# Performance work log

Hardware: AMD Instinct MI355X
Metric: run time of the kernel (lower is better)

The kernel has to match this reference:

```python
import jax, jax.numpy as jnp
import numpy as np

EPS = 1e-6


def _min_max_norm(v):
    # torch: 2.0 + (v - v.min()) / (v.max() - v.min()), global scalars
    mn, mx = v.min(), v.max()
    return 2.0 + (v - mn) / (mx - mn)


def setup_inputs() -> dict:
    key = jax.random.key(0)
    k1, k2, k3 = jax.random.split(key, 3)
    B, C, H, W = 2, 32, 96, 128
    return {
        "queries": jax.random.normal(k1, (B, C, H, W), jnp.float32),
        "keys": jax.random.normal(k2, (B, C, H, W), jnp.float32),
        "values": jax.random.normal(k3, (B, C, H, W), jnp.float32),
    }


def reference(queries, keys, values):
    B, C, H, W = queries.shape

    def row_column_softmax(s):  # s: [B,C,H,W]
        rc = jax.nn.softmax(s, axis=3) + jax.nn.softmax(s, axis=2)
        return rc / rc.max()

    def per_channel(q_c):  # q_c: [B,H,W] -> one output channel
        q = jnp.broadcast_to(q_c[:, None], (B, C, H, W))  # repeat over C
        # q_k_transpose: [B,C,H,H] (einsum sums w and y independently)
        hxh = jnp.einsum('bchw,bcxy->bchx', q, keys) + EPS
        # q_transpose_k: [B,C,W,W]
        wxw = jnp.einsum('bchw,bcxy->bcwy', q, keys) + EPS
        h_row = _min_max_norm(hxh.sum(axis=2))  # [B,C,H]  ('bcij->bcj')
        h_col = _min_max_norm(hxh.sum(axis=3))  # [B,C,H]  ('bcij->bci')
        w_row = _min_max_norm(wxw.sum(axis=2))  # [B,C,W]
        w_col = _min_max_norm(wxw.sum(axis=3))  # [B,C,W]
        outer = lambda m, n: jnp.einsum('bch,bcw->bchw', m, n)
        score = (row_column_softmax(outer(h_row, w_row))
                 + row_column_softmax(outer(h_row, w_col))
                 + row_column_softmax(outer(h_col, w_row))
                 + row_column_softmax(outer(h_col, w_col)))
        score = score / score.max()
        z_c = jnp.einsum('bchw,bchw->bhw', score, values)  # [B,H,W]
        return z_c, score

    # vectorize the original Python loop over query channels
    z_all, scores = jax.vmap(per_channel)(jnp.moveaxis(queries, 1, 0))
    z = jnp.swapaxes(z_all, 0, 1)  # [B,C,H,W]
    # torch returns the atten_score of the LAST loop iteration
    return z, scores[-1]
```

## Files before the change

### kernel.cpp

```cpp
#include <hip/hip_runtime.h>
#include <float.h>

#define BB 2
#define CC 32
#define HH 96
#define WW 128
#define HW (HH*WW)
#define BC (BB*CC)
#define NPLANE (BC*HW)
#define EPSF 1e-6f
#define LOG2E 1.4426950408889634f

#define QR_OFF 0
#define QC_OFF (QR_OFF + BC*HH)
#define QS_OFF (QC_OFF + BC*WW)
#define KR_OFF (QS_OFF + BC)
#define KC_OFF (KR_OFF + BC*HH)
#define KS_OFF (KC_OFF + BC*WW)
#define REC_OFF (KS_OFF + BC)
#define RECSZ 1344
#define BMX_OFF (REC_OFF + CC*BC*RECSZ)
#define BSX_OFF (BMX_OFF + CC*BC*4)

__device__ __forceinline__ float rcpf(float x) { return __builtin_amdgcn_rcpf(x); }
__device__ __forceinline__ float e2(float x) { return __builtin_amdgcn_exp2f(x); }

typedef _Float16 h2v __attribute__((ext_vector_type(2)));
__device__ __forceinline__ unsigned pkrtz_u(float a, float b) {
  return __builtin_bit_cast(unsigned, __builtin_amdgcn_cvt_pkrtz(a, b));
}
__device__ __forceinline__ unsigned pk_add(unsigned a, unsigned b) {
  unsigned d; asm("v_pk_add_f16 %0, %1, %2" : "=v"(d) : "v"(a), "v"(b)); return d;
}
__device__ __forceinline__ unsigned pk_mul(unsigned a, unsigned b) {
  unsigned d; asm("v_pk_mul_f16 %0, %1, %2" : "=v"(d) : "v"(a), "v"(b)); return d;
}
__device__ __forceinline__ unsigned pk_max(unsigned a, unsigned b) {
  unsigned d; asm("v_pk_max_f16 %0, %1, %2" : "=v"(d) : "v"(a), "v"(b)); return d;
}
__device__ __forceinline__ float dot2acc(unsigned u, float acc) {
#if __has_builtin(__builtin_amdgcn_fdot2)
  h2v a = __builtin_bit_cast(h2v, u);
  h2v one = {(_Float16)1.0f, (_Float16)1.0f};
  return __builtin_amdgcn_fdot2(a, one, acc, false);
#else
  float lo = (float)__builtin_bit_cast(_Float16, (unsigned short)(u & 0xffff));
  float hi = (float)__builtin_bit_cast(_Float16, (unsigned short)(u >> 16));
  return acc + lo + hi;
#endif
}
__device__ __forceinline__ float h2max_f(unsigned u) {
  float lo = (float)__builtin_bit_cast(_Float16, (unsigned short)(u & 0xffff));
  float hi = (float)__builtin_bit_cast(_Float16, (unsigned short)(u >> 16));
  return fmaxf(lo, hi);
}

__device__ __forceinline__ float blkmax4(float v) {
  __shared__ float sred[4];
  #pragma unroll
  for (int o = 32; o > 0; o >>= 1) v = fmaxf(v, __shfl_xor(v, o, 64));
  if ((threadIdx.x & 63) == 0) sred[threadIdx.x >> 6] = v;
  __syncthreads();
  float r = fmaxf(fmaxf(sred[0], sred[1]), fmaxf(sred[2], sred[3]));
  __syncthreads();
  return r;
}

__global__ __launch_bounds__(256) void k1_plane_sums(const float* __restrict__ q,
                                                     const float* __restrict__ k,
                                                     float* __restrict__ ws) {
  int pb = blockIdx.x;
  int plane = pb & (BC - 1);
  const float* src = (pb < BC ? q : k) + (size_t)plane * HW;
  float* rowO = ws + (pb < BC ? QR_OFF : KR_OFF) + plane * HH;
  float* colO = ws + (pb < BC ? QC_OFF : KC_OFF) + plane * WW;
  float* totO = ws + (pb < BC ? QS_OFF : KS_OFF) + plane;
  __shared__ float cp[4 * WW];
  __shared__ float rsh[HH];
  __shared__ float wtot[2];
  int tid = threadIdx.x;
  int u = tid >> 6, l = tid & 63;
  float csum0 = 0.f, csum1 = 0.f;
  #pragma unroll 4
  for (int r = 0; r < 24; ++r) {
    int h = u * 24 + r;
    float v0 = src[h * WW + l];
    float v1 = src[h * WW + l + 64];
    csum0 += v0; csum1 += v1;
    float rs = v0 + v1;
    #pragma unroll
    for (int o = 1; o < 64; o <<= 1) rs += __shfl_xor(rs, o, 64);
    if (l == 0) { rowO[h] = rs; rsh[h] = rs; }
  }
  cp[u * WW + l] = csum0;
  cp[u * WW + l + 64] = csum1;
  __syncthreads();
  if (tid < WW) colO[tid] = cp[tid] + cp[WW + tid] + cp[2 * WW + tid] + cp[3 * WW + tid];
  float tv = (tid < HH) ? rsh[tid] : 0.f;
  if (tid < 128) {
    #pragma unroll
    for (int o = 1; o < 64; o <<= 1) tv += __shfl_xor(tv, o, 64);
    if ((tid & 63) == 0) wtot[tid >> 6] = tv;
  }
  __syncthreads();
  if (tid == 0) *totO = wtot[0] + wtot[1];
}

__device__ __forceinline__ float k2_raw(const float* __restrict__ ws, int type, int c0, int i, int L) {
  int bc = i / L, x = i - bc * L;
  int b = bc >> 5;
  if (type == 0) return ws[QS_OFF + b * CC + c0] * ws[KR_OFF + bc * HH + x] + HH * EPSF;
  if (type == 1) return ws[QR_OFF + (b * CC + c0) * HH + x] * ws[KS_OFF + bc] + HH * EPSF;
  if (type == 2) return ws[QS_OFF + b * CC + c0] * ws[KC_OFF + bc * WW + x] + WW * EPSF;
  return ws[QC_OFF + (b * CC + c0) * WW + x] * ws[KS_OFF + bc] + WW * EPSF;
}

__global__ __launch_bounds__(256) void k2_vec_norm(float* __restrict__ ws) {
  int c0 = blockIdx.x >> 2, type = blockIdx.x & 3;
  int L = (type < 2) ? HH : WW;
  int N = BC * L;
  int tid = threadIdx.x;
  float mx = -FLT_MAX, mn = FLT_MAX;
  for (int i = tid; i < N; i += 256) {
    float v = k2_raw(ws, type, c0, i, L);
    mx = fmaxf(mx, v); mn = fminf(mn, v);
  }
  mx = blkmax4(mx);
  mn = -blkmax4(-mn);
  float scale = rcpf(mx - mn);
  float fold = (type < 2) ? LOG2E : 1.0f;
  int fieldbase = (type == 0) ? 0 : (type == 1) ? 96 : (type == 2) ? 192 : 320;
  for (int i = tid; i < N; i += 256) {
    int bc = i / L, x = i - bc * L;
    float v = k2_raw(ws, type, c0, i, L);
    ws[REC_OFF + (size_t)(c0 * BC + bc) * RECSZ + fieldbase + x] =
        (2.0f + (v - mn) * scale) * fold;
  }
}

#define EPH 136
__global__ __launch_bounds__(256) void k3_rc(float* __restrict__ ws) {
  int g = blockIdx.x;
  int vb = g >> 2, t = g & 3;
  float* rec = ws + REC_OFF + (size_t)vb * RECSZ;
  int tid = threadIdx.x;
  int u = tid >> 6, l = tid & 63;
  __shared__ __align__(16) unsigned short eh[HH * EPH];
  __shared__ __align__(16) float mncp[512];
  __shared__ __align__(16) unsigned short rch[128];
  __shared__ float wmx[3];
  const float* mv = rec + (t >> 1) * 96;
  const float* nv = rec + 192 + (t & 1) * 128;
  if (tid < 224) mncp[tid] = (tid < 96) ? mv[tid] : nv[tid - 96];
  __syncthreads();
  float n0 = mncp[96 + 2 * l], n1 = mncp[96 + 2 * l + 1];
  float cs0 = 0.f, cs1 = 0.f;
  #pragma unroll 6
  for (int r = 0; r < 24; ++r) {
    int h = u * 24 + r;
    float m = mncp[h];
    float e0 = e2(m * n0);
    float e1 = e2(m * n1);
    cs0 += e0; cs1 += e1;
    *(unsigned*)&eh[h * EPH + 2 * l] = pkrtz_u(e0, e1);
  }
  __syncthreads();
  mncp[u * 128 + 2 * l] = cs0;
  mncp[u * 128 + 2 * l + 1] = cs1;
  __syncthreads();
  if (tid < 64) {
    int w0 = 2 * tid, w1 = w0 + 1;
    float rc0 = rcpf(mncp[w0] + mncp[128 + w0] + mncp[256 + w0] + mncp[384 + w0]);
    float rc1 = rcpf(mncp[w1] + mncp[128 + w1] + mncp[256 + w1] + mncp[384 + w1]);
    rec[832 + 4 * w0 + t] = rc0;
    rec[832 + 4 * w1 + t] = rc1;
    ((unsigned*)rch)[tid] = pkrtz_u(rc0 * 4096.f, rc1 * 4096.f);
  }
  __syncthreads();
  float mx = 0.f;
  if (tid < 192) {
    int row = tid >> 1, hf = tid & 1;
    const uint4* ep = (const uint4*)&eh[row * EPH + hf * 64];
    float s = 0.f;
    #pragma unroll
    for (int j = 0; j < 8; ++j) {
      uint4 ev = ep[j];
      s = dot2acc(ev.x, s); s = dot2acc(ev.y, s);
      s = dot2acc(ev.z, s); s = dot2acc(ev.w, s);
    }
    s += __shfl_xor(s, 1, 64);
    float rr = rcpf(s);
    if (hf == 0) rec[448 + 4 * row + t] = rr;
    unsigned rr2 = pkrtz_u(rr * 4096.f, rr * 4096.f);
    unsigned mxu = 0;
    const uint4* cp2 = (const uint4*)&rch[hf * 64];
    #pragma unroll
    for (int j = 0; j < 8; ++j) {
      uint4 ev = ep[j];
      uint4 cv = cp2[j];
      mxu = pk_max(mxu, pk_mul(ev.x, pk_add(cv.x, rr2)));
      mxu = pk_max(mxu, pk_mul(ev.y, pk_add(cv.y, rr2)));
      mxu = pk_max(mxu, pk_mul(ev.z, pk_add(cv.z, rr2)));
      mxu = pk_max(mxu, pk_mul(ev.w, pk_add(cv.w, rr2)));
    }
    mx = h2max_f(mxu) * (1.0f / 4096.f);
    #pragma unroll
    for (int o = 1; o < 64; o <<= 1) mx = fmaxf(mx, __shfl_xor(mx, o, 64));
    if ((tid & 63) == 0) wmx[tid >> 6] = mx;
  }
  __syncthreads();
  if (tid == 0) ws[BMX_OFF + vb * 4 + t] = fmaxf(fmaxf(wmx[0], wmx[1]), wmx[2]);
}

#define ELEMS 2
#define TILES 24
#define GRP 4
__global__ __launch_bounds__(256) void k4_score(const float* __restrict__ values,
                                                float* __restrict__ ws,
                                                float* __restrict__ out) {
  int bx = blockIdx.x;
  int tile = bx % TILES;
  int cb = bx / TILES;
  int b = cb & 1, c0 = cb >> 1;
  int tid = threadIdx.x;
  int base = tile * 512;
  int w = tid & 127;
  __shared__ __align__(16) float nS[GRP][256];
  __shared__ __align__(16) float c4S[GRP][512];
  __shared__ __align__(16) float mrf[CC * 24];
  __shared__ float s44[4][4];
  const float* rec0 = ws + REC_OFF + (size_t)(c0 * BC + b * CC) * RECSZ;
  float bm = ws[BMX_OFF + c0 * 256 + tid];
  #pragma unroll
  for (int o = 4; o <= 32; o <<= 1) bm = fmaxf(bm, __shfl_xor(bm, o, 64));
  if ((tid & 63) < 4) s44[tid >> 6][tid & 3] = bm;
  if (tid < 192) {
    int ch = tid / 6, f = tid - 6 * (tid / 6);
    const float* rsrc = rec0 + (size_t)ch * RECSZ;
    int soff = (f == 0) ? tile * 4 : (f == 1) ? 96 + tile * 4 : 448 + 16 * tile + 4 * (f - 2);
    *(float4*)&mrf[ch * 24 + f * 4] = *(const float4*)(rsrc + soff);
  }
  const float* vsrc0 = values + (size_t)(b * CC) * HW + base + tid;
  float v0 = vsrc0[0], v1 = vsrc0[256];
  __syncthreads();
  float im0 = rcpf(fmaxf(fmaxf(s44[0][0], s44[1][0]), fmaxf(s44[2][0], s44[3][0])));
  float im1 = rcpf(fmaxf(fmaxf(s44[0][1], s44[1][1]), fmaxf(s44[2][1], s44[3][1])));
  float im2 = rcpf(fmaxf(fmaxf(s44[0][2], s44[1][2]), fmaxf(s44[2][2], s44[3][2])));
  float im3 = rcpf(fmaxf(fmaxf(s44[0][3], s44[1][3]), fmaxf(s44[2][3], s44[3][3])));
  for (int i = tid; i < CC * 16; i += 256) {
    int ch = i >> 4, kk = i & 15, tt = kk & 3;
    float sel = tt == 0 ? im0 : tt == 1 ? im1 : tt == 2 ? im2 : im3;
    mrf[ch * 24 + 8 + kk] *= sel;
  }
  #pragma unroll
  for (int i = tid; i < GRP * 192; i += 256) {
    int chl = i / 192, rem = i - 192 * (i / 192);
    const float* rsrc = rec0 + (size_t)chl * RECSZ;
    if (rem < 64) {
      *(float4*)&nS[chl][4 * rem] = *(const float4*)(rsrc + 192 + 4 * rem);
    } else {
      float4 g4 = *(const float4*)(rsrc + 832 + 4 * (rem - 64));
      g4.x *= im0; g4.y *= im1; g4.z *= im2; g4.w *= im3;
      *(float4*)&c4S[chl][4 * (rem - 64)] = g4;
    }
  }
  __syncthreads();
  int r0 = tid >> 7;
  float U0 = 0.f, U1 = 0.f, smaxl = 0.f;
  for (int c = 0; c < CC; ++c) {
    if ((c & (GRP - 1)) == 0 && c) {
      __syncthreads();
      #pragma unroll
      for (int i = tid; i < GRP * 192; i += 256) {
        int chl = i / 192, rem = i - 192 * (i / 192);
        const float* rsrc = rec0 + (size_t)(c + chl) * RECSZ;
        if (rem < 64) {
          *(float4*)&nS[chl][4 * rem] = *(const float4*)(rsrc + 192 + 4 * rem);
        } else {
          float4 g4 = *(const float4*)(rsrc + 832 + 4 * (rem - 64));
          g4.x *= im0; g4.y *= im1; g4.z *= im2; g4.w *= im3;
          *(float4*)&c4S[chl][4 * (rem - 64)] = g4;
        }
      }
      __syncthreads();
    }
    float nv0 = 0.f, nv1 = 0.f;
    if (c + 1 < CC) {
      nv0 = vsrc0[(size_t)(c + 1) * HW];
      nv1 = vsrc0[(size_t)(c + 1) * HW + 256];
    }
    int cl = c & (GRP - 1);
    float nr = nS[cl][w], nc = nS[cl][128 + w];
    float4 c4 = *(const float4*)&c4S[cl][4 * w];
    const float* mc = &mrf[c * 24];
    #pragma unroll
    for (int j = 0; j < ELEMS; ++j) {
      int r = r0 + 2 * j;
      float mR = mc[r], mC = mc[4 + r];
      float4 r4 = *(const float4*)&mc[8 + 4 * r];
      float sc = e2(mR * nr) * (r4.x + c4.x) + e2(mR * nc) * (r4.y + c4.y)
               + e2(mC * nr) * (r4.z + c4.z) + e2(mC * nc) * (r4.w + c4.w);
      smaxl = fmaxf(smaxl, sc);
      float uv = sc * (j == 0 ? v0 : v1);
      if (j == 0) U0 += uv; else U1 += uv;
    }
    v0 = nv0; v1 = nv1;
  }
  float* zout = out + (size_t)(b * CC + c0) * HW + base + tid;
  zout[0] = U0;
  zout[256] = U1;
  smaxl = blkmax4(smaxl);
  if (tid == 0) ws[BSX_OFF + bx] = smaxl;
}

#define K5_ZB (BC * 8)
__global__ __launch_bounds__(256) void k5_final(float* __restrict__ out,
                                                const float* __restrict__ ws) {
  int bx = blockIdx.x;
  int tid = threadIdx.x;
  if (bx < K5_ZB) {
    int p = bx >> 3, sub = bx & 7;
    int c0 = p & (CC - 1);
    __shared__ float sm;
    if (tid < 64) {
      float a = (tid < 48) ? ws[BSX_OFF + c0 * 48 + tid] : 0.f;
      #pragma unroll
      for (int o = 1; o < 64; o <<= 1) a = fmaxf(a, __shfl_xor(a, o, 64));
      if (tid == 0) sm = a;
    }
    __syncthreads();
    float ism = rcpf(sm);
    int off = p * HW + sub * 1536 + tid;
    #pragma unroll
    for (int j = 0; j < 6; ++j) out[off + 256 * j] *= ism;
  } else {
    int sp = bx - K5_ZB;
    int plane = sp >> 1, half = sp & 1;
    const float* rec = ws + REC_OFF + (size_t)((CC - 1) * BC + plane) * RECSZ;
    __shared__ __align__(16) float R[RECSZ];
    __shared__ float s44[4][4];
    __shared__ float sm;
    for (int i = tid; i < RECSZ / 4; i += 256) ((float4*)R)[i] = ((const float4*)rec)[i];
    float bm = ws[BMX_OFF + (CC - 1) * 256 + tid];
    #pragma unroll
    for (int o = 4; o <= 32; o <<= 1) bm = fmaxf(bm, __shfl_xor(bm, o, 64));
    if ((tid & 63) < 4) s44[tid >> 6][tid & 3] = bm;
    if (tid < 64) {
      float a = (tid < 48) ? ws[BSX_OFF + (CC - 1) * 48 + tid] : 0.f;
      #pragma unroll
      for (int o = 1; o < 64; o <<= 1) a = fmaxf(a, __shfl_xor(a, o, 64));
      if (tid == 0) sm = a;
    }
    __syncthreads();
    float im0 = rcpf(fmaxf(fmaxf(s44[0][0], s44[1][0]), fmaxf(s44[2][0], s44[3][0])));
    float im1 = rcpf(fmaxf(fmaxf(s44[0][1], s44[1][1]), fmaxf(s44[2][1], s44[3][1])));
    float im2 = rcpf(fmaxf(fmaxf(s44[0][2], s44[1][2]), fmaxf(s44[2][2], s44[3][2])));
    float im3 = rcpf(fmaxf(fmaxf(s44[0][3], s44[1][3]), fmaxf(s44[2][3], s44[3][3])));
    float isml = rcpf(sm);
    float* sout = out + (size_t)NPLANE + (size_t)plane * HW + half * 6144;
    #pragma unroll 4
    for (int e = tid; e < 6144; e += 256) {
      int idx = half * 6144 + e;
      int h = idx >> 7, ww = idx & 127;
      float mR = R[h], mC = R[96 + h];
      float nr = R[192 + ww], nc = R[320 + ww];
      float4 r4 = *(const float4*)&R[448 + 4 * h];
      float4 c4 = *(const float4*)&R[832 + 4 * ww];
      float A0 = c4.x * im0, A1 = c4.y * im1, A2 = c4.z * im2, A3 = c4.w * im3;
      float sc = e2(mR * nr) * fmaf(r4.x, im0, A0) + e2(mR * nc) * fmaf(r4.y, im1, A1)
               + e2(mC * nr) * fmaf(r4.z, im2, A2) + e2(mC * nc) * fmaf(r4.w, im3, A3);
      sout[e] = sc * isml;
    }
  }
}

extern "C" void kernel_launch(void* const* d_in, const int* in_sizes, int n_in,
                              void* d_out, int out_size, void* d_ws, size_t ws_size,
                              hipStream_t stream) {
  const float* q = (const float*)d_in[0];
  const float* k = (const float*)d_in[1];
  const float* v = (const float*)d_in[2];
  float* out = (float*)d_out;
  float* ws = (float*)d_ws;
  k1_plane_sums<<<2 * BC, 256, 0, stream>>>(q, k, ws);
  k2_vec_norm<<<CC * 4, 256, 0, stream>>>(ws);
  k3_rc<<<CC * BC * 4, 256, 0, stream>>>(ws);
  k4_score<<<CC * BB * TILES, 256, 0, stream>>>(v, ws, out);
  k5_final<<<K5_ZB + 128, 256, 0, stream>>>(out, ws);
}
```

Measured before the change: 99.83 us.

## Split k4 channel reduction in two groups with wider pixel tiles per block

k4_score now gives each block half of the 32 value channels and twice as many pixels (four elements per thread instead of two). The grid size stays the same. The second channel group writes its partial z into workspace, and k5_final adds it to the first group's result before scaling by the global max. The aim is to halve the serial channel loop and the LDS refills per block, and to reuse each loaded column factor across four rows for more instruction-level parallelism. The cost is an extra full-size global write and read of partial sums, plus more registers per thread.

```diff
diff --git a/kernel.cpp b/kernel.cpp
--- a/kernel.cpp
+++ b/kernel.cpp
@@ -21,6 +21,7 @@
 #define RECSZ 1344
 #define BMX_OFF (REC_OFF + CC*BC*RECSZ)
 #define BSX_OFF (BMX_OFF + CC*BC*4)
+#define PZ_OFF (BSX_OFF + 1536)
 
 __device__ __forceinline__ float rcpf(float x) { return __builtin_amdgcn_rcpf(x); }
 __device__ __forceinline__ float e2(float x) { return __builtin_amdgcn_exp2f(x); }
@@ -212,50 +213,58 @@
   if (tid == 0) ws[BMX_OFF + vb * 4 + t] = fmaxf(fmaxf(wmx[0], wmx[1]), wmx[2]);
 }
 
-#define ELEMS 2
-#define TILES 24
+#define ELEMS 4
+#define TILES 12
+#define NCG 2
+#define CG (CC/NCG)
 #define GRP 4
 __global__ __launch_bounds__(256) void k4_score(const float* __restrict__ values,
                                                 float* __restrict__ ws,
                                                 float* __restrict__ out) {
   int bx = blockIdx.x;
-  int tile = bx % TILES;
-  int cb = bx / TILES;
+  int cg = bx & 1, bxx = bx >> 1;
+  int tile = bxx % TILES;
+  int cb = bxx / TILES;
   int b = cb & 1, c0 = cb >> 1;
   int tid = threadIdx.x;
-  int base = tile * 512;
-  int w = tid & 127;
+  int base = tile * 1024;
+  int w = tid & 127, r0 = tid >> 7;
   __shared__ __align__(16) float nS[GRP][256];
   __shared__ __align__(16) float c4S[GRP][512];
-  __shared__ __align__(16) float mrf[CC * 24];
+  __shared__ __align__(16) float mrf[CG * 48];
   __shared__ float s44[4][4];
   const float* rec0 = ws + REC_OFF + (size_t)(c0 * BC + b * CC) * RECSZ;
+  const float* recg = rec0 + (size_t)(cg * CG) * RECSZ;
   float bm = ws[BMX_OFF + c0 * 256 + tid];
   #pragma unroll
   for (int o = 4; o <= 32; o <<= 1) bm = fmaxf(bm, __shfl_xor(bm, o, 64));
   if ((tid & 63) < 4) s44[tid >> 6][tid & 3] = bm;
   if (tid < 192) {
-    int ch = tid / 6, f = tid - 6 * (tid / 6);
-    const float* rsrc = rec0 + (size_t)ch * RECSZ;
-    int soff = (f == 0) ? tile * 4 : (f == 1) ? 96 + tile * 4 : 448 + 16 * tile + 4 * (f - 2);
-    *(float4*)&mrf[ch * 24 + f * 4] = *(const float4*)(rsrc + soff);
+    int ch = tid / 12, f = tid - 12 * (tid / 12);
+    const float* rsrc = recg + (size_t)ch * RECSZ;
+    int soff = (f < 2) ? tile * 8 + 4 * f
+             : (f < 4) ? 96 + tile * 8 + 4 * (f - 2)
+                       : 448 + 32 * tile + 4 * (f - 4);
+    *(float4*)&mrf[ch * 48 + f * 4] = *(const float4*)(rsrc + soff);
   }
   const float* vsrc0 = values + (size_t)(b * CC) * HW + base + tid;
-  float v0 = vsrc0[0], v1 = vsrc0[256];
+  float vr[ELEMS];
+  #pragma unroll
+  for (int j = 0; j < ELEMS; ++j) vr[j] = vsrc0[(size_t)(cg * CG) * HW + 256 * j];
   __syncthreads();
   float im0 = rcpf(fmaxf(fmaxf(s44[0][0], s44[1][0]), fmaxf(s44[2][0], s44[3][0])));
   float im1 = rcpf(fmaxf(fmaxf(s44[0][1], s44[1][1]), fmaxf(s44[2][1], s44[3][1])));
   float im2 = rcpf(fmaxf(fmaxf(s44[0][2], s44[1][2]), fmaxf(s44[2][2], s44[3][2])));
   float im3 = rcpf(fmaxf(fmaxf(s44[0][3], s44[1][3]), fmaxf(s44[2][3], s44[3][3])));
-  for (int i = tid; i < CC * 16; i += 256) {
-    int ch = i >> 4, kk = i & 15, tt = kk & 3;
+  for (int i = tid; i < CG * 32; i += 256) {
+    int ch = i >> 5, kk = i & 31, tt = kk & 3;
     float sel = tt == 0 ? im0 : tt == 1 ? im1 : tt == 2 ? im2 : im3;
-    mrf[ch * 24 + 8 + kk] *= sel;
+    mrf[ch * 48 + 16 + kk] *= sel;
   }
   #pragma unroll
   for (int i = tid; i < GRP * 192; i += 256) {
     int chl = i / 192, rem = i - 192 * (i / 192);
-    const float* rsrc = rec0 + (size_t)chl * RECSZ;
+    const float* rsrc = recg + (size_t)chl * RECSZ;
     if (rem < 64) {
       *(float4*)&nS[chl][4 * rem] = *(const float4*)(rsrc + 192 + 4 * rem);
     } else {
@@ -265,15 +274,15 @@
     }
   }
   __syncthreads();
-  int r0 = tid >> 7;
-  float U0 = 0.f, U1 = 0.f, smaxl = 0.f;
-  for (int c = 0; c < CC; ++c) {
-    if ((c & (GRP - 1)) == 0 && c) {
+  float U[ELEMS] = {0.f, 0.f, 0.f, 0.f};
+  float smaxl = 0.f;
+  for (int ci = 0; ci < CG; ++ci) {
+    if ((ci & (GRP - 1)) == 0 && ci) {
       __syncthreads();
       #pragma unroll
       for (int i = tid; i < GRP * 192; i += 256) {
         int chl = i / 192, rem = i - 192 * (i / 192);
-        const float* rsrc = rec0 + (size_t)(c + chl) * RECSZ;
+        const float* rsrc = recg + (size_t)(ci + chl) * RECSZ;
         if (rem < 64) {
           *(float4*)&nS[chl][4 * rem] = *(const float4*)(rsrc + 192 + 4 * rem);
         } else {
@@ -284,31 +293,34 @@
       }
       __syncthreads();
     }
-    float nv0 = 0.f, nv1 = 0.f;
-    if (c + 1 < CC) {
-      nv0 = vsrc0[(size_t)(c + 1) * HW];
-      nv1 = vsrc0[(size_t)(c + 1) * HW + 256];
-    }
-    int cl = c & (GRP - 1);
+    float nv[ELEMS];
+    if (ci + 1 < CG) {
+      #pragma unroll
+      for (int j = 0; j < ELEMS; ++j)
+        nv[j] = vsrc0[(size_t)(cg * CG + ci + 1) * HW + 256 * j];
+    }
+    int cl = ci & (GRP - 1);
     float nr = nS[cl][w], nc = nS[cl][128 + w];
     float4 c4 = *(const float4*)&c4S[cl][4 * w];
-    const float* mc = &mrf[c * 24];
+    const float* mc = &mrf[ci * 48];
     #pragma unroll
     for (int j = 0; j < ELEMS; ++j) {
       int r = r0 + 2 * j;
-      float mR = mc[r], mC = mc[4 + r];
-      float4 r4 = *(const float4*)&mc[8 + 4 * r];
+      float mR = mc[r], mC = mc[8 + r];
+      float4 r4 = *(const float4*)&mc[16 + 4 * r];
       float sc = e2(mR * nr) * (r4.x + c4.x) + e2(mR * nc) * (r4.y + c4.y)
                + e2(mC * nr) * (r4.z + c4.z) + e2(mC * nc) * (r4.w + c4.w);
       smaxl = fmaxf(smaxl, sc);
-      float uv = sc * (j == 0 ? v0 : v1);
-      if (j == 0) U0 += uv; else U1 += uv;
-    }
-    v0 = nv0; v1 = nv1;
-  }
-  float* zout = out + (size_t)(b * CC + c0) * HW + base + tid;
-  zout[0] = U0;
-  zout[256] = U1;
+      U[j] += sc * vr[j];
+    }
+    if (ci + 1 < CG) {
+      #pragma unroll
+      for (int j = 0; j < ELEMS; ++j) vr[j] = nv[j];
+    }
+  }
+  float* zt = (cg == 0 ? out : ws + PZ_OFF) + (size_t)(b * CC + c0) * HW + base + tid;
+  #pragma unroll
+  for (int j = 0; j < ELEMS; ++j) zt[256 * j] = U[j];
   smaxl = blkmax4(smaxl);
   if (tid == 0) ws[BSX_OFF + bx] = smaxl;
 }
@@ -330,9 +342,13 @@
     }
     __syncthreads();
     float ism = rcpf(sm);
+    const float* pz = ws + PZ_OFF;
     int off = p * HW + sub * 1536 + tid;
     #pragma unroll
-    for (int j = 0; j < 6; ++j) out[off + 256 * j] *= ism;
+    for (int j = 0; j < 6; ++j) {
+      int i = off + 256 * j;
+      out[i] = (out[i] + pz[i]) * ism;
+    }
   } else {
     int sp = bx - K5_ZB;
     int plane = sp >> 1, half = sp & 1;
@@ -385,6 +401,6 @@
   k1_plane_sums<<<2 * BC, 256, 0, stream>>>(q, k, ws);
   k2_vec_norm<<<CC * 4, 256, 0, stream>>>(ws);
   k3_rc<<<CC * BC * 4, 256, 0, stream>>>(ws);
-  k4_score<<<CC * BB * TILES, 256, 0, stream>>>(v, ws, out);
+  k4_score<<<CC * BB * TILES * NCG, 256, 0, stream>>>(v, ws, out);
   k5_final<<<K5_ZB + 128, 256, 0, stream>>>(out, ws);
 }
```

After: 98.27 us (median of 2 runs). No clear change (-1.6%).
